# Kernel optimization log

Hardware: AMD Instinct MI355X
Metric: run time of the kernel (lower is better)

The kernel has to match this reference:

```python
import jax, jax.numpy as jnp
import numpy as np

TEMPERATURE = 0.1

def setup_inputs() -> dict:
    key = jax.random.key(0)
    k1, k2 = jax.random.split(key)
    B, D, NUM_CLASSES = 4096, 512, 64
    emb = jax.random.normal(k1, (B, D), dtype=jnp.float32)
    # L2-normalize so sims/temperature stays in a safe range for exp()
    emb = emb / jnp.linalg.norm(emb, axis=1, keepdims=True)
    labels = jax.random.randint(k2, (B,), 0, NUM_CLASSES, dtype=jnp.int64)
    return {"embeddings": emb, "labels": labels}

def reference(embeddings, labels):
    B = embeddings.shape[0]
    # [B, B] similarity matrix, scaled by temperature
    sims = jnp.matmul(embeddings, embeddings.T) / TEMPERATURE
    same = labels[:, None] == labels[None, :]
    eye = jnp.eye(B, dtype=bool)
    pos_mask = (same & ~eye).astype(sims.dtype)   # positives, diagonal excluded
    neg_mask = (~same).astype(sims.dtype)          # negatives
    exp_s = jnp.exp(sims)
    # denominator[i] = sum over negatives of exp_s[i, :]
    denom = jnp.sum(exp_s * neg_mask, axis=1, keepdims=True)  # [B, 1]
    # per positive pair (i, j): -log(exp_s[i,j] / (denom[i] + exp_s[i,j]))
    per_pair = -jnp.log(exp_s / (denom + exp_s))
    loss_sum = jnp.sum(per_pair * pos_mask)
    num_pos = jnp.sum(pos_mask)
    return loss_sum / jnp.maximum(num_pos, 1.0)
```

## Files before the change

kernel.cpp:

```cpp
#include <hip/hip_runtime.h>
#include <hip/hip_bf16.h>

#define B_N 4096
#define D_K 512
#define INV_T 10.0f

#define BM 128
#define CPB 256
#define CS (B_N/CPB)
#define NT 16
#define NJT (CPB/NT)
#define SLOTS 12


typedef __attribute__((ext_vector_type(8))) short short8;
typedef __attribute__((ext_vector_type(4))) float float4v;

static __device__ inline unsigned short f32_to_bf16_rne(float f) {
    unsigned int u = __float_as_uint(f);
    unsigned int lsb = (u >> 16) & 1u;
    u += 0x7fffu + lsb;
    return (unsigned short)(u >> 16);
}

__global__ __launch_bounds__(256) void k0_convert(const float* __restrict__ emb,
                                                  unsigned short* __restrict__ embB) {
    int tid = blockIdx.x * 256 + threadIdx.x;
    int base = tid * 4;
    float4 v = *(const float4*)(emb + base);
    ushort4 o;
    o.x = f32_to_bf16_rne(v.x);
    o.y = f32_to_bf16_rne(v.y);
    o.z = f32_to_bf16_rne(v.z);
    o.w = f32_to_bf16_rne(v.w);
    *(ushort4*)(embB + base) = o;
}

__global__ __launch_bounds__(256, 2) void k1_denom(const unsigned short* __restrict__ embB,
                                                   const int* __restrict__ labels,
                                                   float* __restrict__ denomPart,
                                                   int* __restrict__ posCnt,
                                                   float* __restrict__ posS) {
    __shared__ unsigned short sB[16 * 512];
    __shared__ float sPos[BM * SLOTS];
    __shared__ int   sCnt[BM];

    const int tid  = threadIdx.x;
    const int wave = tid >> 6;
    const int lane = tid & 63;
    const int quad = lane >> 4;
    const int l16  = lane & 15;
    const int by   = blockIdx.y;

    const int rowBase  = blockIdx.x * BM;
    const int colBase0 = by * CPB;

    if (tid < BM) sCnt[tid] = 0;

    short8 afrag[2][16];
#pragma unroll
    for (int t = 0; t < 2; ++t) {
        const unsigned short* ap = embB + (rowBase + wave * 32 + t * 16 + l16) * D_K + quad * 8;
#pragma unroll
        for (int kc = 0; kc < 16; ++kc)
            afrag[t][kc] = *(const short8*)(ap + kc * 32);
    }

    int labI[2][4];
#pragma unroll
    for (int t = 0; t < 2; ++t)
#pragma unroll
        for (int r = 0; r < 4; ++r)
            labI[t][r] = labels[rowBase + wave * 32 + t * 16 + quad * 4 + r];

    float rowAcc[2][4] = {{0.f,0.f,0.f,0.f},{0.f,0.f,0.f,0.f}};

    for (int jt = 0; jt < NJT; ++jt) {
        const int colBase = colBase0 + jt * NT;

        __syncthreads();
#pragma unroll
        for (int p = 0; p < 4; ++p) {
            int li = p * 256 + tid;
            int c  = li >> 6;
            int j  = li & 63;
            short8 v = *(const short8*)(embB + (colBase + c) * D_K + j * 8);
            *(short8*)(sB + (c * 64 + (j ^ (c & 7))) * 8) = v;
        }
        __syncthreads();

        float4v acc[2];
        acc[0] = (float4v){0.f, 0.f, 0.f, 0.f};
        acc[1] = (float4v){0.f, 0.f, 0.f, 0.f};
#pragma unroll
        for (int kc = 0; kc < 16; ++kc) {
            int j = kc * 4 + quad;
            short8 bfrag = *(const short8*)(sB + (l16 * 64 + (j ^ (l16 & 7))) * 8);
            acc[0] = __builtin_amdgcn_mfma_f32_16x16x32_bf16(afrag[0][kc], bfrag, acc[0], 0, 0, 0);
            acc[1] = __builtin_amdgcn_mfma_f32_16x16x32_bf16(afrag[1][kc], bfrag, acc[1], 0, 0, 0);
        }

        const int labJ = labels[colBase + l16];
        const int col  = colBase + l16;
#pragma unroll
        for (int t = 0; t < 2; ++t) {
#pragma unroll
            for (int r = 0; r < 4; ++r) {
                float s = acc[t][r] * INV_T;
                const int lr = wave * 32 + t * 16 + quad * 4 + r;
                if (labJ != labI[t][r]) {
                    rowAcc[t][r] += __expf(s);
                } else if (col != rowBase + lr) {
                    int idx = atomicAdd(&sCnt[lr], 1);
                    if (idx < SLOTS) sPos[lr * SLOTS + idx] = s;
                }
            }
        }
    }

#pragma unroll
    for (int t = 0; t < 2; ++t)
#pragma unroll
        for (int r = 0; r < 4; ++r) {
            float v = rowAcc[t][r];
            v += __shfl_xor(v, 1);
            v += __shfl_xor(v, 2);
            v += __shfl_xor(v, 4);
            v += __shfl_xor(v, 8);
            if (l16 == 0)
                denomPart[(rowBase + wave * 32 + t * 16 + quad * 4 + r) * CS + by] = v;
        }

    __syncthreads();
    if (tid < BM) {
        const int c   = min(sCnt[tid], SLOTS);
        const int row = rowBase + tid;
        posCnt[row * CS + by] = c;
        for (int m = 0; m < c; ++m)
            posS[(row * CS + by) * SLOTS + m] = sPos[tid * SLOTS + m];
    }
}

__global__ __launch_bounds__(256) void k2_pos(const float* __restrict__ denomPart,
                                              const int* __restrict__ posCnt,
                                              const float* __restrict__ posS,
                                              float* __restrict__ termSum,
                                              float* __restrict__ cntF) {
    const int wave = threadIdx.x >> 6;
    const int lane = threadIdx.x & 63;
    const int i    = blockIdx.x * 4 + wave;

    float d = (lane < CS) ? denomPart[i * CS + lane] : 0.0f;
    float c = (lane < CS) ? (float)posCnt[i * CS + lane] : 0.0f;
#pragma unroll
    for (int off = 32; off; off >>= 1) {
        d += __shfl_xor(d, off);
        c += __shfl_xor(c, off);
    }

    float sum = 0.0f;
#pragma unroll
    for (int it = 0; it < 3; ++it) {
        int slot = lane + it * 64;
        int b    = slot / SLOTS;
        int m    = slot - b * SLOTS;
        int cb   = posCnt[i * CS + b];
        if (m < cb) {
            float s = posS[i * CS * SLOTS + slot];
            sum += __logf(d + __expf(s)) - s;
        }
    }
#pragma unroll
    for (int off = 32; off; off >>= 1) sum += __shfl_xor(sum, off);
    if (lane == 0) { termSum[i] = sum; cntF[i] = c; }
}

__global__ __launch_bounds__(256) void k3_final(const float* __restrict__ termSum,
                                                const float* __restrict__ cntF,
                                                float* __restrict__ out) {
    __shared__ float sL[256], sC[256];
    float ls = 0.0f, cs = 0.0f;
    for (int i = threadIdx.x; i < B_N; i += 256) { ls += termSum[i]; cs += cntF[i]; }
    sL[threadIdx.x] = ls; sC[threadIdx.x] = cs;
    __syncthreads();
    for (int s = 128; s; s >>= 1) {
        if (threadIdx.x < s) {
            sL[threadIdx.x] += sL[threadIdx.x + s];
            sC[threadIdx.x] += sC[threadIdx.x + s];
        }
        __syncthreads();
    }
    if (threadIdx.x == 0) out[0] = sL[0] / fmaxf(sC[0], 1.0f);
}

extern "C" void kernel_launch(void* const* d_in, const int* in_sizes, int n_in,
                              void* d_out, int out_size, void* d_ws, size_t ws_size,
                              hipStream_t stream) {
    const float* emb    = (const float*)d_in[0];
    const int*   labels = (const int*)d_in[1];
    float*       out    = (float*)d_out;

    char* ws = (char*)d_ws;
    float*          termSum   = (float*)(ws);
    float*          cntF      = (float*)(ws + 16384);
    float*          denomPart = (float*)(ws + 32768);
    int*            posCnt    = (int*)(ws + 294912);
    float*          posS      = (float*)(ws + 557056);
    unsigned short* embB      = (unsigned short*)(ws + (4u << 20));

    k0_convert<<<dim3(B_N * D_K / 4 / 256), dim3(256), 0, stream>>>(emb, embB);

    k1_denom<<<dim3(B_N / BM, CS), dim3(256), 0, stream>>>(embB, labels, denomPart, posCnt, posS);

    k2_pos<<<dim3(B_N / 4), dim3(256), 0, stream>>>(denomPart, posCnt, posS, termSum, cntF);

    k3_final<<<dim3(1), dim3(256), 0, stream>>>(termSum, cntF, out);
}
```

Measured before the change: 110.0 us.

## Exploit symmetry of similarity matrix: compute upper-triangle tiles only, scatter column results

Each 128x128 tile block now processes only tiles with J>=I and contributes both row sums and transposed column sums of negative exps and positive entries. This removes nearly half of the MFMA and exp work, at the cost of extra shared-memory column accumulation, more atomics, and wider per-row partial buffers. The B-tile staging is also switched to direct global-to-LDS loads. Half the launched blocks exit immediately, and the load per block is now uneven.

```diff
diff --git a/kernel.cpp b/kernel.cpp
--- a/kernel.cpp
+++ b/kernel.cpp
@@ -5,12 +5,11 @@
 #define D_K 512
 #define INV_T 10.0f
 
-#define BM 128
-#define CPB 256
-#define CS (B_N/CPB)
+#define TILE 128
+#define NTG (B_N / TILE)
 #define NT 16
-#define NJT (CPB/NT)
-#define SLOTS 12
+#define NJT (TILE / NT)
+#define SLOTS 16
 
 
 typedef __attribute__((ext_vector_type(8))) short short8;
@@ -42,20 +41,27 @@
                                                    int* __restrict__ posCnt,
                                                    float* __restrict__ posS) {
     __shared__ unsigned short sB[16 * 512];
-    __shared__ float sPos[BM * SLOTS];
-    __shared__ int   sCnt[BM];
+    __shared__ float sColAccW[4][TILE];
+    __shared__ float sPosR[TILE * SLOTS];
+    __shared__ float sPosC[TILE * SLOTS];
+    __shared__ int   sCntR[TILE];
+    __shared__ int   sCntC[TILE];
+
+    const int I = blockIdx.y, J = blockIdx.x;
+    if (J < I) return;
+    const bool diag = (I == J);
 
     const int tid  = threadIdx.x;
     const int wave = tid >> 6;
     const int lane = tid & 63;
     const int quad = lane >> 4;
     const int l16  = lane & 15;
-    const int by   = blockIdx.y;
-
-    const int rowBase  = blockIdx.x * BM;
-    const int colBase0 = by * CPB;
-
-    if (tid < BM) sCnt[tid] = 0;
+
+    const int rowBase  = I * TILE;
+    const int colBase0 = J * TILE;
+
+    if (tid < TILE) { sCntR[tid] = 0; sCntC[tid] = 0; }
+    for (int x = lane; x < TILE; x += 64) sColAccW[wave][x] = 0.0f;
 
     short8 afrag[2][16];
 #pragma unroll
@@ -81,11 +87,12 @@
         __syncthreads();
 #pragma unroll
         for (int p = 0; p < 4; ++p) {
-            int li = p * 256 + tid;
-            int c  = li >> 6;
-            int j  = li & 63;
-            short8 v = *(const short8*)(embB + (colBase + c) * D_K + j * 8);
-            *(short8*)(sB + (c * 64 + (j ^ (c & 7))) * 8) = v;
+            const int c = p * 4 + wave;
+            const unsigned short* gp = embB + (colBase + c) * D_K + (lane ^ (c & 7)) * 8;
+            __builtin_amdgcn_global_load_lds(
+                (const __attribute__((address_space(1))) unsigned int*)gp,
+                (__attribute__((address_space(3))) unsigned int*)(sB + c * 64 * 8),
+                16, 0, 0);
         }
         __syncthreads();
 
@@ -102,19 +109,33 @@
 
         const int labJ = labels[colBase + l16];
         const int col  = colBase + l16;
+        float colLocal = 0.0f;
 #pragma unroll
         for (int t = 0; t < 2; ++t) {
 #pragma unroll
             for (int r = 0; r < 4; ++r) {
                 float s = acc[t][r] * INV_T;
-                const int lr = wave * 32 + t * 16 + quad * 4 + r;
-                if (labJ != labI[t][r]) {
-                    rowAcc[t][r] += __expf(s);
-                } else if (col != rowBase + lr) {
-                    int idx = atomicAdd(&sCnt[lr], 1);
-                    if (idx < SLOTS) sPos[lr * SLOTS + idx] = s;
+                const int lr  = wave * 32 + t * 16 + quad * 4 + r;
+                const int row = rowBase + lr;
+                const bool neg = (labJ != labI[t][r]);
+                float e = neg ? __expf(s) : 0.0f;
+                rowAcc[t][r] += e;
+                colLocal     += e;
+                if (!neg && col != row) {
+                    int idx = atomicAdd(&sCntR[lr], 1);
+                    if (idx < SLOTS) sPosR[lr * SLOTS + idx] = s;
+                    if (!diag) {
+                        const int lc = jt * NT + l16;
+                        int idx2 = atomicAdd(&sCntC[lc], 1);
+                        if (idx2 < SLOTS) sPosC[lc * SLOTS + idx2] = s;
+                    }
                 }
             }
+        }
+        if (!diag) {
+            colLocal += __shfl_xor(colLocal, 16);
+            colLocal += __shfl_xor(colLocal, 32);
+            if (quad == 0) sColAccW[wave][jt * NT + l16] += colLocal;
         }
     }
 
@@ -128,16 +149,26 @@
             v += __shfl_xor(v, 4);
             v += __shfl_xor(v, 8);
             if (l16 == 0)
-                denomPart[(rowBase + wave * 32 + t * 16 + quad * 4 + r) * CS + by] = v;
+                denomPart[(rowBase + wave * 32 + t * 16 + quad * 4 + r) * 64 + J] = v;
         }
 
     __syncthreads();
-    if (tid < BM) {
-        const int c   = min(sCnt[tid], SLOTS);
-        const int row = rowBase + tid;
-        posCnt[row * CS + by] = c;
+
+    if (!diag && tid < TILE) {
+        float cs = sColAccW[0][tid] + sColAccW[1][tid] + sColAccW[2][tid] + sColAccW[3][tid];
+        const int rowJ = colBase0 + tid;
+        denomPart[rowJ * 64 + 32 + I] = cs;
+        const int c = min(sCntC[tid], SLOTS);
+        posCnt[rowJ * 64 + 32 + I] = c;
         for (int m = 0; m < c; ++m)
-            posS[(row * CS + by) * SLOTS + m] = sPos[tid * SLOTS + m];
+            posS[(rowJ * 64 + 32 + I) * SLOTS + m] = sPosC[tid * SLOTS + m];
+    }
+    if (tid < TILE) {
+        const int rowI = rowBase + tid;
+        const int c = min(sCntR[tid], SLOTS);
+        posCnt[rowI * 64 + J] = c;
+        for (int m = 0; m < c; ++m)
+            posS[(rowI * 64 + J) * SLOTS + m] = sPosR[tid * SLOTS + m];
     }
 }
 
@@ -149,9 +180,12 @@
     const int wave = threadIdx.x >> 6;
     const int lane = threadIdx.x & 63;
     const int i    = blockIdx.x * 4 + wave;
-
-    float d = (lane < CS) ? denomPart[i * CS + lane] : 0.0f;
-    float c = (lane < CS) ? (float)posCnt[i * CS + lane] : 0.0f;
+    const int m    = i >> 7;
+
+    const bool valid = (lane < 32) ? (lane >= m) : (lane - 32 < m);
+    float d  = valid ? denomPart[i * 64 + lane] : 0.0f;
+    int   cb = valid ? posCnt[i * 64 + lane]    : 0;
+    float c  = (float)cb;
 #pragma unroll
     for (int off = 32; off; off >>= 1) {
         d += __shfl_xor(d, off);
@@ -159,14 +193,11 @@
     }
 
     float sum = 0.0f;
-#pragma unroll
-    for (int it = 0; it < 3; ++it) {
-        int slot = lane + it * 64;
-        int b    = slot / SLOTS;
-        int m    = slot - b * SLOTS;
-        int cb   = posCnt[i * CS + b];
-        if (m < cb) {
-            float s = posS[i * CS * SLOTS + slot];
+    const float* ps = posS + (i * 64 + lane) * SLOTS;
+#pragma unroll
+    for (int m2 = 0; m2 < SLOTS; ++m2) {
+        if (m2 < cb) {
+            float s = ps[m2];
             sum += __logf(d + __expf(s)) - s;
         }
     }
@@ -204,13 +235,13 @@
     float*          termSum   = (float*)(ws);
     float*          cntF      = (float*)(ws + 16384);
     float*          denomPart = (float*)(ws + 32768);
-    int*            posCnt    = (int*)(ws + 294912);
-    float*          posS      = (float*)(ws + 557056);
-    unsigned short* embB      = (unsigned short*)(ws + (4u << 20));
+    int*            posCnt    = (int*)(ws + 1081344);
+    float*          posS      = (float*)(ws + 2129920);
+    unsigned short* embB      = (unsigned short*)(ws + 20971520);
 
     k0_convert<<<dim3(B_N * D_K / 4 / 256), dim3(256), 0, stream>>>(emb, embB);
 
-    k1_denom<<<dim3(B_N / BM, CS), dim3(256), 0, stream>>>(embB, labels, denomPart, posCnt, posS);
+    k1_denom<<<dim3(NTG, NTG), dim3(256), 0, stream>>>(embB, labels, denomPart, posCnt, posS);
 
     k2_pos<<<dim3(B_N / 4), dim3(256), 0, stream>>>(denomPart, posCnt, posS, termSum, cntF);
 
```

Result: slower. 121.4 us (+10.4%).

## Pre-tile bf16 embeddings into MFMA fragment layout and drop LDS staging

Applied to the files above, without the earlier changes.

The convert kernel now writes bf16 embeddings in a fragment-major layout, so each lane's MFMA operand is one contiguous 16-byte load. The main kernel reads B fragments straight from global memory/L2 instead of staging 16-column tiles through swizzled LDS, which removes two __syncthreads per column tile. The positive-slot count per row and block goes from 12 to 16 so indexing in the reduction uses shifts, at the cost of a larger posS buffer. Each wave now issues its own global loads for shared B data, which increases L2 traffic and leaves no LDS reuse across the four waves.

```diff
diff --git a/kernel.cpp b/kernel.cpp
--- a/kernel.cpp
+++ b/kernel.cpp
@@ -7,10 +7,8 @@
 
 #define BM 128
 #define CPB 256
-#define CS (B_N/CPB)
-#define NT 16
-#define NJT (CPB/NT)
-#define SLOTS 12
+#define CS (B_N / CPB)
+#define SLOTS 16
 
 
 typedef __attribute__((ext_vector_type(8))) short short8;
@@ -24,24 +22,28 @@
 }
 
 __global__ __launch_bounds__(256) void k0_convert(const float* __restrict__ emb,
-                                                  unsigned short* __restrict__ embB) {
+                                                  unsigned short* __restrict__ embT) {
     int tid = blockIdx.x * 256 + threadIdx.x;
-    int base = tid * 4;
-    float4 v = *(const float4*)(emb + base);
-    ushort4 o;
-    o.x = f32_to_bf16_rne(v.x);
-    o.y = f32_to_bf16_rne(v.y);
-    o.z = f32_to_bf16_rne(v.z);
-    o.w = f32_to_bf16_rne(v.w);
-    *(ushort4*)(embB + base) = o;
-}
-
-__global__ __launch_bounds__(256, 2) void k1_denom(const unsigned short* __restrict__ embB,
+    int row = tid >> 6;
+    int kq  = tid & 63;
+    const float* sp = emb + row * D_K + kq * 8;
+    float4 v0 = *(const float4*)(sp);
+    float4 v1 = *(const float4*)(sp + 4);
+    ushort4 o0, o1;
+    o0.x = f32_to_bf16_rne(v0.x); o0.y = f32_to_bf16_rne(v0.y);
+    o0.z = f32_to_bf16_rne(v0.z); o0.w = f32_to_bf16_rne(v0.w);
+    o1.x = f32_to_bf16_rne(v1.x); o1.y = f32_to_bf16_rne(v1.y);
+    o1.z = f32_to_bf16_rne(v1.z); o1.w = f32_to_bf16_rne(v1.w);
+    unsigned short* dp = embT + (((row >> 4) * 64 + kq) * 16 + (row & 15)) * 8;
+    *(ushort4*)(dp)     = o0;
+    *(ushort4*)(dp + 4) = o1;
+}
+
+__global__ __launch_bounds__(256, 2) void k1_denom(const unsigned short* __restrict__ embT,
                                                    const int* __restrict__ labels,
                                                    float* __restrict__ denomPart,
                                                    int* __restrict__ posCnt,
                                                    float* __restrict__ posS) {
-    __shared__ unsigned short sB[16 * 512];
     __shared__ float sPos[BM * SLOTS];
     __shared__ int   sCnt[BM];
 
@@ -50,20 +52,20 @@
     const int lane = tid & 63;
     const int quad = lane >> 4;
     const int l16  = lane & 15;
-    const int by   = blockIdx.y;
-
-    const int rowBase  = blockIdx.x * BM;
-    const int colBase0 = by * CPB;
+    const int bx   = blockIdx.x, by = blockIdx.y;
+
+    const int rowBase = bx * BM;
 
     if (tid < BM) sCnt[tid] = 0;
 
     short8 afrag[2][16];
 #pragma unroll
     for (int t = 0; t < 2; ++t) {
-        const unsigned short* ap = embB + (rowBase + wave * 32 + t * 16 + l16) * D_K + quad * 8;
+        const int g = bx * 8 + wave * 2 + t;
+        const unsigned short* ap = embT + (g * 64 * 16 + lane) * 8;
 #pragma unroll
         for (int kc = 0; kc < 16; ++kc)
-            afrag[t][kc] = *(const short8*)(ap + kc * 32);
+            afrag[t][kc] = *(const short8*)(ap + kc * 4 * 16 * 8);
     }
 
     int labI[2][4];
@@ -73,41 +75,32 @@
         for (int r = 0; r < 4; ++r)
             labI[t][r] = labels[rowBase + wave * 32 + t * 16 + quad * 4 + r];
 
+    __syncthreads();
+
     float rowAcc[2][4] = {{0.f,0.f,0.f,0.f},{0.f,0.f,0.f,0.f}};
 
-    for (int jt = 0; jt < NJT; ++jt) {
-        const int colBase = colBase0 + jt * NT;
-
-        __syncthreads();
-#pragma unroll
-        for (int p = 0; p < 4; ++p) {
-            int li = p * 256 + tid;
-            int c  = li >> 6;
-            int j  = li & 63;
-            short8 v = *(const short8*)(embB + (colBase + c) * D_K + j * 8);
-            *(short8*)(sB + (c * 64 + (j ^ (c & 7))) * 8) = v;
-        }
-        __syncthreads();
+    for (int cg = 0; cg < CPB / 16; ++cg) {
+        const int g2 = by * 16 + cg;
+        const unsigned short* bp = embT + (g2 * 64 * 16 + lane) * 8;
 
         float4v acc[2];
         acc[0] = (float4v){0.f, 0.f, 0.f, 0.f};
         acc[1] = (float4v){0.f, 0.f, 0.f, 0.f};
 #pragma unroll
         for (int kc = 0; kc < 16; ++kc) {
-            int j = kc * 4 + quad;
-            short8 bfrag = *(const short8*)(sB + (l16 * 64 + (j ^ (l16 & 7))) * 8);
+            short8 bfrag = *(const short8*)(bp + kc * 4 * 16 * 8);
             acc[0] = __builtin_amdgcn_mfma_f32_16x16x32_bf16(afrag[0][kc], bfrag, acc[0], 0, 0, 0);
             acc[1] = __builtin_amdgcn_mfma_f32_16x16x32_bf16(afrag[1][kc], bfrag, acc[1], 0, 0, 0);
         }
 
-        const int labJ = labels[colBase + l16];
-        const int col  = colBase + l16;
+        const int col  = g2 * 16 + l16;
+        const int labJ = labels[col];
 #pragma unroll
         for (int t = 0; t < 2; ++t) {
 #pragma unroll
             for (int r = 0; r < 4; ++r) {
                 float s = acc[t][r] * INV_T;
-                const int lr = wave * 32 + t * 16 + quad * 4 + r;
+                const int lr  = wave * 32 + t * 16 + quad * 4 + r;
                 if (labJ != labI[t][r]) {
                     rowAcc[t][r] += __expf(s);
                 } else if (col != rowBase + lr) {
@@ -133,8 +126,8 @@
 
     __syncthreads();
     if (tid < BM) {
+        const int row = rowBase + tid;
         const int c   = min(sCnt[tid], SLOTS);
-        const int row = rowBase + tid;
         posCnt[row * CS + by] = c;
         for (int m = 0; m < c; ++m)
             posS[(row * CS + by) * SLOTS + m] = sPos[tid * SLOTS + m];
@@ -160,10 +153,10 @@
 
     float sum = 0.0f;
 #pragma unroll
-    for (int it = 0; it < 3; ++it) {
+    for (int it = 0; it < (CS * SLOTS) / 64; ++it) {
         int slot = lane + it * 64;
-        int b    = slot / SLOTS;
-        int m    = slot - b * SLOTS;
+        int b    = slot >> 4;
+        int m    = slot & 15;
         int cb   = posCnt[i * CS + b];
         if (m < cb) {
             float s = posS[i * CS * SLOTS + slot];
@@ -206,11 +199,11 @@
     float*          denomPart = (float*)(ws + 32768);
     int*            posCnt    = (int*)(ws + 294912);
     float*          posS      = (float*)(ws + 557056);
-    unsigned short* embB      = (unsigned short*)(ws + (4u << 20));
-
-    k0_convert<<<dim3(B_N * D_K / 4 / 256), dim3(256), 0, stream>>>(emb, embB);
-
-    k1_denom<<<dim3(B_N / BM, CS), dim3(256), 0, stream>>>(embB, labels, denomPart, posCnt, posS);
+    unsigned short* embT      = (unsigned short*)(ws + 8388608);
+
+    k0_convert<<<dim3(B_N * D_K / 8 / 256), dim3(256), 0, stream>>>(emb, embT);
+
+    k1_denom<<<dim3(B_N / BM, CS), dim3(256), 0, stream>>>(embT, labels, denomPart, posCnt, posS);
 
     k2_pos<<<dim3(B_N / 4), dim3(256), 0, stream>>>(denomPart, posCnt, posS, termSum, cntF);
 
```

New measurement: 116.1 us. 1.06x slower.
